# Kernel tuning notes

Hardware: AMD Instinct MI355X
Metric: run time of the kernel (lower is better)

The kernel has to match this reference:

```python
import jax, jax.numpy as jnp
import numpy as np

N_MODEL = 1024
N_HEADS = 16
KV_HEADS = 4
HEAD_DIM = N_MODEL // N_HEADS          # 64
KV_MODEL = HEAD_DIM * KV_HEADS         # 256
GROUPS = N_HEADS // KV_HEADS           # 4
B, S = 4, 2048


def _rmsnorm(x):
    return x * jax.lax.rsqrt(jnp.mean(x * x, axis=-1, keepdims=True) + 1e-6)


def _act_quant(x):
    # 8-bit absmax per-token quantization (BitNet b1.58)
    scale = 127.0 / jnp.clip(jnp.max(jnp.abs(x), axis=-1, keepdims=True), 1e-5)
    return jnp.clip(jnp.round(x * scale), -128.0, 127.0) / scale


def _weight_quant(w):
    # ternary absmean quantization
    scale = 1.0 / jnp.clip(jnp.mean(jnp.abs(w)), 1e-5)
    return jnp.clip(jnp.round(w * scale), -1.0, 1.0) / scale


def bitlinear(x, w, b):
    xn = _rmsnorm(x)
    xq = xn + jax.lax.stop_gradient(_act_quant(xn) - xn)   # STE
    wq = w + jax.lax.stop_gradient(_weight_quant(w) - w)   # STE
    return jnp.einsum('...i,oi->...o', xq, wq) + b


def setup_inputs() -> dict:
    key = jax.random.key(0)
    ks = jax.random.split(key, 11)
    sq = 1.0 / np.sqrt(N_MODEL)
    sk = 1.0 / np.sqrt(KV_MODEL)
    return {
        'query': jax.random.normal(ks[0], (B, S, N_MODEL), jnp.float32),
        'key':   jax.random.normal(ks[1], (B, S, N_MODEL), jnp.float32),
        'value': jax.random.normal(ks[2], (B, S, N_MODEL), jnp.float32),
        'Wq': jax.random.normal(ks[3], (N_MODEL, N_MODEL), jnp.float32) * sq,
        'bq': jnp.zeros((N_MODEL,), jnp.float32),
        'Wk': jax.random.normal(ks[4], (KV_MODEL, N_MODEL), jnp.float32) * sq,
        'bk': jnp.zeros((KV_MODEL,), jnp.float32),
        'Wv': jax.random.normal(ks[5], (KV_MODEL, N_MODEL), jnp.float32) * sq,
        'bv': jnp.zeros((KV_MODEL,), jnp.float32),
        'Wo': jax.random.normal(ks[6], (N_MODEL, KV_MODEL), jnp.float32) * sk,
        'bo': jnp.zeros((N_MODEL,), jnp.float32),
    }


def reference(query, key, value, Wq, bq, Wk, bk, Wv, bv, Wo, bo):
    b = query.shape[0]
    Q = bitlinear(query, Wq, bq)   # [b, n, n_model]
    K = bitlinear(key,   Wk, bk)   # [b, s, kv_model]
    V = bitlinear(value, Wv, bv)   # [b, s, kv_model]

    # [b, h, n, d] layouts
    Q = Q.reshape(b, -1, N_HEADS, HEAD_DIM).transpose(0, 2, 1, 3)
    K = K.reshape(b, -1, KV_HEADS, HEAD_DIM).transpose(0, 2, 1, 3)
    V = V.reshape(b, -1, KV_HEADS, HEAD_DIM).transpose(0, 2, 1, 3)

    # group query heads: [b, g, kv_h, n, d]
    Qg = Q.reshape(b, KV_HEADS, GROUPS, -1, HEAD_DIM).transpose(0, 2, 1, 3, 4)
    # NOTE: faithful to the module, the einsum output has no 'g' axis,
    # so the grouped query heads are SUMMED over g.
    energy = jnp.einsum('bghnd,bhsd->bhns', Qg, K)  # [b, kv_h, n, s]

    scale = jnp.sqrt(jnp.float32(HEAD_DIM))
    attention = jax.nn.softmax(energy / scale, axis=-1)
    x = jnp.einsum('bhns,bhsd->bhnd', attention, V)  # [b, kv_h, n, d]
    x = x.transpose(0, 2, 1, 3).reshape(b, -1, KV_MODEL)
    x = bitlinear(x, Wo, bo)       # [b, n, n_model]
    return (x, attention)
```

## Files before the change

kernel.cpp:

```cpp
#include <hip/hip_runtime.h>
#include <stdint.h>

#define N_MODELC 1024
#define KV_MODELC 256
#define BATCH 4
#define SEQ 2048
#define NTOK (BATCH*SEQ)

typedef __attribute__((ext_vector_type(4))) float f32x4;
typedef __attribute__((ext_vector_type(4))) int   i32x4;
typedef __attribute__((ext_vector_type(8))) short s16x8;

#define LOG2E 1.4426950408889634f
#define PSHIFT 32.0f

__device__ __forceinline__ unsigned short f2bf(float f){
  unsigned u = __builtin_bit_cast(unsigned, f);
  u = (u + 0x7FFFu + ((u>>16)&1u)) >> 16;
  return (unsigned short)u;
}
__device__ __forceinline__ float bf2f(unsigned short b){
  return __builtin_bit_cast(float, ((unsigned)b)<<16);
}

__global__ __launch_bounds__(256) void k_actquant1024(
    const float* __restrict__ xq_in, const float* __restrict__ xk_in, const float* __restrict__ xv_in,
    int8_t* __restrict__ q8q, int8_t* __restrict__ q8k, int8_t* __restrict__ q8v,
    float* __restrict__ scq, float* __restrict__ sck, float* __restrict__ scv)
{
  int row = blockIdx.x, which = blockIdx.y, t = threadIdx.x;
  const float* x = (which==0)?xq_in:(which==1)?xk_in:xv_in;
  int8_t* q8 = (which==0)?q8q:(which==1)?q8k:q8v;
  float* sc = (which==0)?scq:(which==1)?sck:scv;
  const float* xr = x + (size_t)row*N_MODELC;
  float4 v = reinterpret_cast<const float4*>(xr)[t];
  float ss = v.x*v.x + v.y*v.y + v.z*v.z + v.w*v.w;
  float am = fmaxf(fmaxf(fabsf(v.x),fabsf(v.y)), fmaxf(fabsf(v.z),fabsf(v.w)));
  #pragma unroll
  for (int m=32;m;m>>=1){ ss += __shfl_xor(ss,m,64); am = fmaxf(am, __shfl_xor(am,m,64)); }
  __shared__ float red[8];
  int wid = t>>6;
  if ((t&63)==0){ red[wid]=ss; red[4+wid]=am; }
  __syncthreads();
  ss = red[0]+red[1]+red[2]+red[3];
  am = fmaxf(fmaxf(red[4],red[5]), fmaxf(red[6],red[7]));
  float rinv = rsqrtf(ss*(1.0f/N_MODELC) + 1e-6f);
  float clipv = fmaxf(am*rinv, 1e-5f);
  float qs = 127.0f/clipv;
  float fsc = rinv*qs;
  char4 o;
  o.x = (signed char)(int)fminf(127.f, fmaxf(-128.f, rintf(v.x*fsc)));
  o.y = (signed char)(int)fminf(127.f, fmaxf(-128.f, rintf(v.y*fsc)));
  o.z = (signed char)(int)fminf(127.f, fmaxf(-128.f, rintf(v.z*fsc)));
  o.w = (signed char)(int)fminf(127.f, fmaxf(-128.f, rintf(v.w*fsc)));
  reinterpret_cast<char4*>(q8 + (size_t)row*N_MODELC)[t] = o;
  if (t==0) sc[row] = clipv*(1.0f/127.0f);
}

__global__ __launch_bounds__(64) void k_actquant256(
    const float* __restrict__ X, int8_t* __restrict__ q8, float* __restrict__ sc)
{
  int row = blockIdx.x, l = threadIdx.x;
  float4 v = reinterpret_cast<const float4*>(X + (size_t)row*KV_MODELC)[l];
  float ss = v.x*v.x + v.y*v.y + v.z*v.z + v.w*v.w;
  float am = fmaxf(fmaxf(fabsf(v.x),fabsf(v.y)), fmaxf(fabsf(v.z),fabsf(v.w)));
  #pragma unroll
  for (int m=32;m;m>>=1){ ss += __shfl_xor(ss,m,64); am = fmaxf(am, __shfl_xor(am,m,64)); }
  float rinv = rsqrtf(ss*(1.0f/KV_MODELC) + 1e-6f);
  float clipv = fmaxf(am*rinv, 1e-5f);
  float qs = 127.0f/clipv;
  float fsc = rinv*qs;
  char4 o;
  o.x = (signed char)(int)fminf(127.f, fmaxf(-128.f, rintf(v.x*fsc)));
  o.y = (signed char)(int)fminf(127.f, fmaxf(-128.f, rintf(v.y*fsc)));
  o.z = (signed char)(int)fminf(127.f, fmaxf(-128.f, rintf(v.z*fsc)));
  o.w = (signed char)(int)fminf(127.f, fmaxf(-128.f, rintf(v.w*fsc)));
  reinterpret_cast<char4*>(q8 + (size_t)row*KV_MODELC)[l] = o;
  if (l==0) sc[row] = clipv*(1.0f/127.0f);
}

__global__ __launch_bounds__(256) void k_wabs_partial(
    const float* __restrict__ Wq, const float* __restrict__ Wk,
    const float* __restrict__ Wv, const float* __restrict__ Wo, float* __restrict__ partial)
{
  int mat = blockIdx.y;
  const float* w = (mat==0)?Wq:(mat==1)?Wk:(mat==2)?Wv:Wo;
  int n = (mat==0)?(N_MODELC*N_MODELC):(KV_MODELC*N_MODELC);
  float s = 0.f;
  for (int i = blockIdx.x*256 + threadIdx.x; i < n; i += 256*256) s += fabsf(w[i]);
  #pragma unroll
  for (int m=32;m;m>>=1) s += __shfl_xor(s,m,64);
  __shared__ float red[4];
  int wid = threadIdx.x>>6;
  if ((threadIdx.x&63)==0) red[wid]=s;
  __syncthreads();
  if (threadIdx.x==0) partial[mat*256 + blockIdx.x] = red[0]+red[1]+red[2]+red[3];
}

__global__ __launch_bounds__(256) void k_wfinal(const float* __restrict__ partial, float* __restrict__ wfac)
{
  int mat = blockIdx.x, t = threadIdx.x;
  float s = partial[mat*256 + t];
  #pragma unroll
  for (int m=32;m;m>>=1) s += __shfl_xor(s,m,64);
  __shared__ float red[4];
  int wid = t>>6;
  if ((t&63)==0) red[wid]=s;
  __syncthreads();
  if (t==0){
    float tot = red[0]+red[1]+red[2]+red[3];
    float n = (mat==0)?(float)(N_MODELC*N_MODELC):(float)(KV_MODELC*N_MODELC);
    wfac[mat] = fmaxf(tot/n, 1e-5f);
  }
}

__global__ __launch_bounds__(256) void k_tern(
    const float* __restrict__ Wq, const float* __restrict__ Wk,
    const float* __restrict__ Wv, const float* __restrict__ Wo,
    const float* __restrict__ wfac,
    int8_t* __restrict__ Wqs, int8_t* __restrict__ Wkt,
    int8_t* __restrict__ Wvt, int8_t* __restrict__ Wot)
{
  int mat = blockIdx.y;
  int idx = blockIdx.x*256 + threadIdx.x;
  if (mat==0){
    float s = 1.0f/wfac[0];
    int op = idx>>10, i = idx&1023;
    int kv = op>>6, d = op&63;
    int acc = 0;
    #pragma unroll
    for (int g=0; g<4; g++){
      float w = Wq[(size_t)(kv*256 + g*64 + d)*N_MODELC + i];
      float r = fminf(1.f, fmaxf(-1.f, rintf(w*s)));
      acc += (int)r;
    }
    Wqs[idx] = (int8_t)acc;
  } else {
    const float* w = (mat==1)?Wk:(mat==2)?Wv:Wo;
    int8_t* o = (mat==1)?Wkt:(mat==2)?Wvt:Wot;
    float s = 1.0f/wfac[mat];
    float r = fminf(1.f, fmaxf(-1.f, rintf(w[idx]*s)));
    o[idx] = (int8_t)r;
  }
}

template<int MODE>
__global__ __launch_bounds__(512) void k_gemm_i8_1024(
    const int8_t* __restrict__ A, const int8_t* __restrict__ B,
    const float* __restrict__ rowscale, const float* __restrict__ wfac, int wfi,
    const float* __restrict__ bias, unsigned short* __restrict__ outp)
{
  __shared__ i32x4 redk[4][4][64];
  __shared__ unsigned short tlds[(MODE==2)?64:1][72];
  const int KDIM = 1024;
  int mb = blockIdx.x*64, nb = blockIdx.y*64;
  int w = threadIdx.x>>6, l = threadIdx.x&63, lr = l&15, lk = l>>4;
  int rw = w&3, kh = w>>2;
  const int8_t* Ap = A + (size_t)(mb + rw*16 + lr)*KDIM + kh*512 + lk*16;
  const int8_t* Bp = B + (size_t)(nb + lr)*KDIM + kh*512 + lk*16;
  i32x4 acc[4];
  #pragma unroll
  for (int f=0; f<4; f++) acc[f] = i32x4{0,0,0,0};
  #pragma unroll 4
  for (int kk=0; kk<512; kk+=64){
    i32x4 a = *reinterpret_cast<const i32x4*>(Ap + kk);
    #pragma unroll
    for (int f=0; f<4; f++){
      i32x4 b = *reinterpret_cast<const i32x4*>(Bp + (size_t)f*16*KDIM + kk);
      acc[f] = __builtin_amdgcn_mfma_i32_16x16x64_i8(a, b, acc[f], 0, 0, 0);
    }
  }
  if (kh==1){
    #pragma unroll
    for (int f=0; f<4; f++) redk[rw][f][l] = acc[f];
  }
  __syncthreads();
  if (kh==0){
    float wf = wfac[wfi];
    #pragma unroll
    for (int f=0; f<4; f++){
      acc[f] += redk[rw][f][l];
      int col = nb + f*16 + lr;
      float bval;
      if constexpr (MODE==0){
        int kv = col>>6, d = col&63;
        const float* bb = bias + kv*256 + d;
        bval = bb[0]+bb[64]+bb[128]+bb[192];
      } else {
        bval = bias[col];
      }
      #pragma unroll
      for (int r=0; r<4; r++){
        int row = mb + rw*16 + lk*4 + r;
        float val = (float)acc[f][r] * (rowscale[row]*wf) + bval;
        if constexpr (MODE==0){
          outp[(size_t)row*KV_MODELC + col] = f2bf(0.125f*val);
        } else if constexpr (MODE==1){
          outp[(size_t)row*KV_MODELC + col] = f2bf(val);
        } else {
          tlds[f*16+lr][rw*16 + lk*4 + r] = f2bf(val);
        }
      }
    }
  }
  if constexpr (MODE==2){
    __syncthreads();
    int u = threadIdx.x;
    int col = u>>3, part = u&7;
    int b = mb>>11, s0 = mb&2047;
    s16x8 vv = *reinterpret_cast<const s16x8*>(&tlds[col][part*8]);
    *reinterpret_cast<s16x8*>(&outp[((size_t)(b*256 + nb + col))*SEQ + s0 + part*8]) = vv;
  }
}

__global__ __launch_bounds__(256) void k_gemm_o(
    const int8_t* __restrict__ A, const int8_t* __restrict__ B,
    const float* __restrict__ rowscale, const float* __restrict__ wfac,
    const float* __restrict__ bias, float* __restrict__ outp)
{
  const int KDIM = 256;
  int mb = blockIdx.x*64, nb = blockIdx.y*64;
  int w = threadIdx.x>>6, l = threadIdx.x&63, lr = l&15, lk = l>>4;
  const int8_t* Ap = A + (size_t)(mb + w*16 + lr)*KDIM + lk*16;
  const int8_t* Bp = B + (size_t)(nb + lr)*KDIM + lk*16;
  i32x4 acc[4];
  #pragma unroll
  for (int f=0; f<4; f++) acc[f] = i32x4{0,0,0,0};
  #pragma unroll
  for (int kk=0; kk<KDIM; kk+=64){
    i32x4 a = *reinterpret_cast<const i32x4*>(Ap + kk);
    #pragma unroll
    for (int f=0; f<4; f++){
      i32x4 b = *reinterpret_cast<const i32x4*>(Bp + (size_t)f*16*KDIM + kk);
      acc[f] = __builtin_amdgcn_mfma_i32_16x16x64_i8(a, b, acc[f], 0, 0, 0);
    }
  }
  float wf = wfac[3];
  #pragma unroll
  for (int f=0; f<4; f++){
    int col = nb + f*16 + lr;
    float bval = bias[col];
    #pragma unroll
    for (int r=0; r<4; r++){
      int row = mb + w*16 + lk*4 + r;
      outp[(size_t)row*N_MODELC + col] = (float)acc[f][r]*(rowscale[row]*wf) + bval;
    }
  }
}

__global__ __launch_bounds__(256) void k_attn_fused(
    const unsigned short* __restrict__ Qs, const unsigned short* __restrict__ Kb,
    const unsigned short* __restrict__ VT, unsigned short* __restrict__ Pws,
    float* __restrict__ attn, float* __restrict__ X)
{
  __shared__ unsigned short plds[64][64];
  __shared__ float linvl[64];
  int bkv = blockIdx.y, b = bkv>>2, kv = bkv&3;
  int w = threadIdx.x>>6, l = threadIdx.x&63, lr = l&15, lk = l>>4;
  int brow = blockIdx.x*64;
  int rowt = brow + w*16;
  size_t tq = (size_t)(b*SEQ + rowt + lr)*KV_MODELC + kv*64 + lk*8;
  s16x8 qa0 = *reinterpret_cast<const s16x8*>(Qs + tq);
  s16x8 qa1 = *reinterpret_cast<const s16x8*>(Qs + tq + 32);
  const unsigned short* kbase = Kb + (size_t)b*SEQ*KV_MODELC + kv*64 + lk*8;
  const unsigned short* vbase = VT + ((size_t)(b*256 + kv*64))*SEQ;
  unsigned short* pblk = Pws + ((size_t)(bkv*32 + blockIdx.x))*64*SEQ;

  s16x8 ones;
  #pragma unroll
  for (int i=0;i<8;i++) ones[i] = (short)0x3F80;

  f32x4 acco[4];
  #pragma unroll
  for (int dt=0; dt<4; dt++) acco[dt] = f32x4{0.f,0.f,0.f,0.f};
  f32x4 accl = {0.f,0.f,0.f,0.f};

  int qw = w*16 + lk*4;
  int qr = w*16 + lr;
  int rsw = (lr&7)<<3;
  int rbrow = w*16 + (l>>2);
  int rbb = l&3;

  for (int st=0; st<SEQ; st+=64){
    #pragma unroll
    for (int sub=0; sub<4; sub++){
      int s0 = st + sub*16;
      const unsigned short* kp = kbase + (size_t)(s0+lr)*KV_MODELC;
      s16x8 k0 = *reinterpret_cast<const s16x8*>(kp);
      s16x8 k1 = *reinterpret_cast<const s16x8*>(kp + 32);
      f32x4 acc = {0.f,0.f,0.f,0.f};
      acc = __builtin_amdgcn_mfma_f32_16x16x32_bf16(qa0, k0, acc, 0,0,0);
      acc = __builtin_amdgcn_mfma_f32_16x16x32_bf16(qa1, k1, acc, 0,0,0);
      int slocal = sub*16 + lr;
      #pragma unroll
      for (int r=0;r<4;r++){
        float p = exp2f(fmaf(acc[r], LOG2E, -PSHIFT));
        int sw = (slocal & 7) | ((((slocal>>3) ^ ((qw+r)&7)))<<3);
        plds[qw + r][sw] = f2bf(p);
      }
    }
    s16x8 a0 = *reinterpret_cast<const s16x8*>(&plds[qr][(lk<<3) ^ rsw]);
    s16x8 a1 = *reinterpret_cast<const s16x8*>(&plds[qr][((4+lk)<<3) ^ rsw]);
    accl = __builtin_amdgcn_mfma_f32_16x16x32_bf16(a0, ones, accl, 0,0,0);
    accl = __builtin_amdgcn_mfma_f32_16x16x32_bf16(a1, ones, accl, 0,0,0);
    #pragma unroll
    for (int dt=0; dt<4; dt++){
      const unsigned short* vp = vbase + (size_t)(dt*16+lr)*SEQ + st + lk*8;
      s16x8 b0 = *reinterpret_cast<const s16x8*>(vp);
      s16x8 b1 = *reinterpret_cast<const s16x8*>(vp + 32);
      acco[dt] = __builtin_amdgcn_mfma_f32_16x16x32_bf16(a0, b0, acco[dt], 0,0,0);
      acco[dt] = __builtin_amdgcn_mfma_f32_16x16x32_bf16(a1, b1, acco[dt], 0,0,0);
    }
    unsigned short* ptile = pblk + (size_t)(st>>6)*4096;
    #pragma unroll
    for (int j8=0; j8<2; j8++){
      int chunk = rbb*2 + j8;
      s16x8 v = *reinterpret_cast<const s16x8*>(&plds[rbrow][(chunk ^ (rbrow&7))<<3]);
      *reinterpret_cast<s16x8*>(&ptile[rbrow*64 + chunk*8]) = v;
    }
  }

  float invr[4];
  #pragma unroll
  for (int r=0;r<4;r++) invr[r] = 1.0f/accl[r];
  if (lr==0){
    #pragma unroll
    for (int r=0;r<4;r++) linvl[w*16 + lk*4 + r] = invr[r];
  }
  int token = b*SEQ + rowt + lk*4;
  #pragma unroll
  for (int dt=0; dt<4; dt++){
    #pragma unroll
    for (int r=0; r<4; r++){
      X[(size_t)(token + r)*KV_MODELC + kv*64 + dt*16 + lr] = acco[dt][r]*invr[r];
    }
  }
  __syncthreads();

  float* arow = attn + (size_t)bkv*SEQ*SEQ + (size_t)brow*SEQ;
  int t = threadIdx.x;
  const unsigned short* prd = pblk + (size_t)(t>>3)*4096 + (t&7)*8;
  #pragma unroll 4
  for (int it=0; it<64; it++){
    float inv = linvl[it];
    s16x8 pv = *reinterpret_cast<const s16x8*>(prd + it*64);
    float4 o0, o1;
    o0.x = bf2f((unsigned short)pv[0])*inv;
    o0.y = bf2f((unsigned short)pv[1])*inv;
    o0.z = bf2f((unsigned short)pv[2])*inv;
    o0.w = bf2f((unsigned short)pv[3])*inv;
    o1.x = bf2f((unsigned short)pv[4])*inv;
    o1.y = bf2f((unsigned short)pv[5])*inv;
    o1.z = bf2f((unsigned short)pv[6])*inv;
    o1.w = bf2f((unsigned short)pv[7])*inv;
    float* dst = &arow[(size_t)it*SEQ + t*8];
    *reinterpret_cast<float4*>(dst) = o0;
    *reinterpret_cast<float4*>(dst+4) = o1;
  }
}

extern "C" void kernel_launch(void* const* d_in, const int* in_sizes, int n_in,
                              void* d_out, int out_size, void* d_ws, size_t ws_size,
                              hipStream_t stream)
{
  (void)in_sizes; (void)n_in; (void)out_size; (void)ws_size;
  const float* q  = (const float*)d_in[0];
  const float* k  = (const float*)d_in[1];
  const float* v  = (const float*)d_in[2];
  const float* Wq = (const float*)d_in[3];
  const float* bq = (const float*)d_in[4];
  const float* Wk = (const float*)d_in[5];
  const float* bk = (const float*)d_in[6];
  const float* Wv = (const float*)d_in[7];
  const float* bv = (const float*)d_in[8];
  const float* Wo = (const float*)d_in[9];
  const float* bo = (const float*)d_in[10];

  float* out_x = (float*)d_out;
  float* out_attn = out_x + (size_t)NTOK*N_MODELC;

  char* ws = (char*)d_ws;
  size_t off = 0;
  auto alloc = [&](size_t bytes)->void*{
    void* p = ws + off; off += (bytes + 255) & ~(size_t)255; return p;
  };
  int8_t* q8q = (int8_t*)alloc((size_t)NTOK*N_MODELC);
  int8_t* q8k = (int8_t*)alloc((size_t)NTOK*N_MODELC);
  int8_t* q8v = (int8_t*)alloc((size_t)NTOK*N_MODELC);
  int8_t* q8x = (int8_t*)alloc((size_t)NTOK*KV_MODELC);
  float* scq = (float*)alloc(NTOK*4);
  float* sck = (float*)alloc(NTOK*4);
  float* scv = (float*)alloc(NTOK*4);
  float* scx = (float*)alloc(NTOK*4);
  float* partial = (float*)alloc(4*256*4);
  float* wfac = (float*)alloc(256);
  int8_t* Wqs = (int8_t*)alloc(256*1024);
  int8_t* Wkt = (int8_t*)alloc(256*1024);
  int8_t* Wvt = (int8_t*)alloc(256*1024);
  int8_t* Wot = (int8_t*)alloc(1024*256);
  unsigned short* Qs = (unsigned short*)alloc((size_t)NTOK*KV_MODELC*2);
  unsigned short* Kb = (unsigned short*)alloc((size_t)NTOK*KV_MODELC*2);
  unsigned short* VT = (unsigned short*)alloc((size_t)NTOK*KV_MODELC*2);
  float* X = (float*)alloc((size_t)NTOK*KV_MODELC*4);
  unsigned short* Pws = (unsigned short*)alloc((size_t)16*SEQ*SEQ*2);

  hipLaunchKernelGGL(k_actquant1024, dim3(NTOK,3), dim3(256), 0, stream,
                     q,k,v, q8q,q8k,q8v, scq,sck,scv);
  hipLaunchKernelGGL(k_wabs_partial, dim3(256,4), dim3(256), 0, stream, Wq,Wk,Wv,Wo, partial);
  hipLaunchKernelGGL(k_wfinal, dim3(4), dim3(256), 0, stream, partial, wfac);
  hipLaunchKernelGGL(k_tern, dim3(1024,4), dim3(256), 0, stream,
                     Wq,Wk,Wv,Wo, wfac, Wqs,Wkt,Wvt,Wot);
  hipLaunchKernelGGL((k_gemm_i8_1024<0>), dim3(128,4), dim3(512), 0, stream,
                     q8q, Wqs, scq, wfac, 0, bq, Qs);
  hipLaunchKernelGGL((k_gemm_i8_1024<1>), dim3(128,4), dim3(512), 0, stream,
                     q8k, Wkt, sck, wfac, 1, bk, Kb);
  hipLaunchKernelGGL((k_gemm_i8_1024<2>), dim3(128,4), dim3(512), 0, stream,
                     q8v, Wvt, scv, wfac, 2, bv, VT);
  hipLaunchKernelGGL(k_attn_fused, dim3(32,16), dim3(256), 0, stream,
                     Qs, Kb, VT, Pws, out_attn, X);
  hipLaunchKernelGGL(k_actquant256, dim3(NTOK), dim3(64), 0, stream, X, q8x, scx);
  hipLaunchKernelGGL(k_gemm_o, dim3(128,16), dim3(256), 0, stream,
                     q8x, Wot, scx, wfac, bo, out_x);
}
```

Measured before the change: 351.4 us.

## Split attention over key chunks and normalize in separate reduction kernels

The fused attention kernel, which ran only 512 blocks, is split along the key dimension into 8 chunks, giving 4096 blocks. Each block writes partial row sums and partial PV accumulators, and unnormalized probabilities go to a row-major bf16 workspace. A new reduction kernel sums the partials to produce X and the inverse row sums, and a second streaming kernel rescales the workspace into the fp32 attention output. The exp2 call is also switched to the hardware builtin. The aim is better GPU occupancy, at the cost of two extra launches and extra global traffic for the partial buffers.

```diff
diff --git a/kernel.cpp b/kernel.cpp
--- a/kernel.cpp
+++ b/kernel.cpp
@@ -6,6 +6,8 @@
 #define BATCH 4
 #define SEQ 2048
 #define NTOK (BATCH*SEQ)
+#define NCHUNK 8
+#define CHUNK (SEQ/NCHUNK)
 
 typedef __attribute__((ext_vector_type(4))) float f32x4;
 typedef __attribute__((ext_vector_type(4))) int   i32x4;
@@ -248,14 +250,15 @@
   }
 }
 
-__global__ __launch_bounds__(256) void k_attn_fused(
+__global__ __launch_bounds__(256) void k_attn_a(
     const unsigned short* __restrict__ Qs, const unsigned short* __restrict__ Kb,
-    const unsigned short* __restrict__ VT, unsigned short* __restrict__ Pws,
-    float* __restrict__ attn, float* __restrict__ X)
+    const unsigned short* __restrict__ VT,
+    unsigned short* __restrict__ Pws, float* __restrict__ lpart,
+    float* __restrict__ pvpart)
 {
   __shared__ unsigned short plds[64][64];
-  __shared__ float linvl[64];
   int bkv = blockIdx.y, b = bkv>>2, kv = bkv&3;
+  int z = blockIdx.z;
   int w = threadIdx.x>>6, l = threadIdx.x&63, lr = l&15, lk = l>>4;
   int brow = blockIdx.x*64;
   int rowt = brow + w*16;
@@ -264,7 +267,6 @@
   s16x8 qa1 = *reinterpret_cast<const s16x8*>(Qs + tq + 32);
   const unsigned short* kbase = Kb + (size_t)b*SEQ*KV_MODELC + kv*64 + lk*8;
   const unsigned short* vbase = VT + ((size_t)(b*256 + kv*64))*SEQ;
-  unsigned short* pblk = Pws + ((size_t)(bkv*32 + blockIdx.x))*64*SEQ;
 
   s16x8 ones;
   #pragma unroll
@@ -281,7 +283,7 @@
   int rbrow = w*16 + (l>>2);
   int rbb = l&3;
 
-  for (int st=0; st<SEQ; st+=64){
+  for (int st=z*CHUNK; st<z*CHUNK+CHUNK; st+=64){
     #pragma unroll
     for (int sub=0; sub<4; sub++){
       int s0 = st + sub*16;
@@ -294,7 +296,7 @@
       int slocal = sub*16 + lr;
       #pragma unroll
       for (int r=0;r<4;r++){
-        float p = exp2f(fmaf(acc[r], LOG2E, -PSHIFT));
+        float p = __builtin_amdgcn_exp2f(fmaf(acc[r], LOG2E, -PSHIFT));
         int sw = (slocal & 7) | ((((slocal>>3) ^ ((qw+r)&7)))<<3);
         plds[qw + r][sw] = f2bf(p);
       }
@@ -311,49 +313,85 @@
       acco[dt] = __builtin_amdgcn_mfma_f32_16x16x32_bf16(a0, b0, acco[dt], 0,0,0);
       acco[dt] = __builtin_amdgcn_mfma_f32_16x16x32_bf16(a1, b1, acco[dt], 0,0,0);
     }
-    unsigned short* ptile = pblk + (size_t)(st>>6)*4096;
+    unsigned short* prow = Pws + ((size_t)(bkv*SEQ) + brow + rbrow)*SEQ + st;
     #pragma unroll
     for (int j8=0; j8<2; j8++){
-      int chunk = rbb*2 + j8;
-      s16x8 v = *reinterpret_cast<const s16x8*>(&plds[rbrow][(chunk ^ (rbrow&7))<<3]);
-      *reinterpret_cast<s16x8*>(&ptile[rbrow*64 + chunk*8]) = v;
-    }
-  }
-
-  float invr[4];
-  #pragma unroll
-  for (int r=0;r<4;r++) invr[r] = 1.0f/accl[r];
+      int c8 = rbb*2 + j8;
+      s16x8 vv = *reinterpret_cast<const s16x8*>(&plds[rbrow][(c8 ^ (rbrow&7))<<3]);
+      *reinterpret_cast<s16x8*>(&prow[c8*8]) = vv;
+    }
+  }
+
   if (lr==0){
     #pragma unroll
-    for (int r=0;r<4;r++) linvl[w*16 + lk*4 + r] = invr[r];
-  }
-  int token = b*SEQ + rowt + lk*4;
-  #pragma unroll
-  for (int dt=0; dt<4; dt++){
-    #pragma unroll
-    for (int r=0; r<4; r++){
-      X[(size_t)(token + r)*KV_MODELC + kv*64 + dt*16 + lr] = acco[dt][r]*invr[r];
-    }
-  }
-  __syncthreads();
-
-  float* arow = attn + (size_t)bkv*SEQ*SEQ + (size_t)brow*SEQ;
+    for (int r=0;r<4;r++)
+      lpart[((size_t)z*16 + bkv)*SEQ + rowt + lk*4 + r] = accl[r];
+  }
+  float* base = pvpart + ((((size_t)z*16 + bkv)*32 + blockIdx.x)*4 + w)*1024;
+  #pragma unroll
+  for (int dt=0; dt<4; dt++)
+    *reinterpret_cast<f32x4*>(base + (dt*64 + l)*4) = acco[dt];
+}
+
+__global__ __launch_bounds__(256) void k_pvnorm(
+    const float* __restrict__ lpart, const float* __restrict__ pvpart,
+    float* __restrict__ invl, float* __restrict__ X)
+{
+  __shared__ float xls[16][65];
+  __shared__ float linv[16];
+  int T = blockIdx.x;
+  int w = T&3, qblk = (T>>2)&31, bkv = T>>7;
+  int b = bkv>>2, kv = bkv&3;
+  int t = threadIdx.x, l = t&63, dt = t>>6, lk = l>>4, lr = l&15;
+  f32x4 s = {0.f,0.f,0.f,0.f};
+  #pragma unroll
+  for (int z=0; z<NCHUNK; z++){
+    f32x4 v = *reinterpret_cast<const f32x4*>(
+        pvpart + ((((size_t)z*16 + bkv)*32 + qblk)*4 + w)*1024 + t*4);
+    s += v;
+  }
+  if (t < 16){
+    int row = qblk*64 + w*16 + t;
+    float ls = 0.f;
+    #pragma unroll
+    for (int z=0; z<NCHUNK; z++) ls += lpart[((size_t)z*16 + bkv)*SEQ + row];
+    float iv = 1.0f/ls;
+    linv[t] = iv;
+    invl[(size_t)bkv*SEQ + row] = iv;
+  }
+  __syncthreads();
+  #pragma unroll
+  for (int r=0; r<4; r++) xls[lk*4+r][dt*16+lr] = s[r]*linv[lk*4+r];
+  __syncthreads();
+  int row = t>>4, col4 = (t&15)*4;
+  float4 o;
+  o.x = xls[row][col4];   o.y = xls[row][col4+1];
+  o.z = xls[row][col4+2]; o.w = xls[row][col4+3];
+  *reinterpret_cast<float4*>(
+      &X[((size_t)(b*SEQ + qblk*64 + w*16 + row))*KV_MODELC + kv*64 + col4]) = o;
+}
+
+__global__ __launch_bounds__(256) void k_pnorm(
+    const unsigned short* __restrict__ Pws, const float* __restrict__ invl,
+    float* __restrict__ attn)
+{
+  size_t base = (size_t)blockIdx.x*32768;
   int t = threadIdx.x;
-  const unsigned short* prd = pblk + (size_t)(t>>3)*4096 + (t&7)*8;
   #pragma unroll 4
-  for (int it=0; it<64; it++){
-    float inv = linvl[it];
-    s16x8 pv = *reinterpret_cast<const s16x8*>(prd + it*64);
+  for (int i=0; i<16; i++){
+    size_t idx = base + (size_t)i*2048 + t*8;
+    float iv = invl[idx>>11];
+    s16x8 pv = *reinterpret_cast<const s16x8*>(&Pws[idx]);
     float4 o0, o1;
-    o0.x = bf2f((unsigned short)pv[0])*inv;
-    o0.y = bf2f((unsigned short)pv[1])*inv;
-    o0.z = bf2f((unsigned short)pv[2])*inv;
-    o0.w = bf2f((unsigned short)pv[3])*inv;
-    o1.x = bf2f((unsigned short)pv[4])*inv;
-    o1.y = bf2f((unsigned short)pv[5])*inv;
-    o1.z = bf2f((unsigned short)pv[6])*inv;
-    o1.w = bf2f((unsigned short)pv[7])*inv;
-    float* dst = &arow[(size_t)it*SEQ + t*8];
+    o0.x = bf2f((unsigned short)pv[0])*iv;
+    o0.y = bf2f((unsigned short)pv[1])*iv;
+    o0.z = bf2f((unsigned short)pv[2])*iv;
+    o0.w = bf2f((unsigned short)pv[3])*iv;
+    o1.x = bf2f((unsigned short)pv[4])*iv;
+    o1.y = bf2f((unsigned short)pv[5])*iv;
+    o1.z = bf2f((unsigned short)pv[6])*iv;
+    o1.w = bf2f((unsigned short)pv[7])*iv;
+    float* dst = &attn[idx];
     *reinterpret_cast<float4*>(dst) = o0;
     *reinterpret_cast<float4*>(dst+4) = o1;
   }
@@ -403,6 +441,9 @@
   unsigned short* VT = (unsigned short*)alloc((size_t)NTOK*KV_MODELC*2);
   float* X = (float*)alloc((size_t)NTOK*KV_MODELC*4);
   unsigned short* Pws = (unsigned short*)alloc((size_t)16*SEQ*SEQ*2);
+  float* lpart = (float*)alloc((size_t)NCHUNK*16*SEQ*4);
+  float* pvpart = (float*)alloc((size_t)NCHUNK*16*32*4*1024*4);
+  float* invl = (float*)alloc((size_t)16*SEQ*4);
 
   hipLaunchKernelGGL(k_actquant1024, dim3(NTOK,3), dim3(256), 0, stream,
                      q,k,v, q8q,q8k,q8v, scq,sck,scv);
@@ -416,8 +457,12 @@
                      q8k, Wkt, sck, wfac, 1, bk, Kb);
   hipLaunchKernelGGL((k_gemm_i8_1024<2>), dim3(128,4), dim3(512), 0, stream,
                      q8v, Wvt, scv, wfac, 2, bv, VT);
-  hipLaunchKernelGGL(k_attn_fused, dim3(32,16), dim3(256), 0, stream,
-                     Qs, Kb, VT, Pws, out_attn, X);
+  hipLaunchKernelGGL(k_attn_a, dim3(32,16,NCHUNK), dim3(256), 0, stream,
+                     Qs, Kb, VT, Pws, lpart, pvpart);
+  hipLaunchKernelGGL(k_pvnorm, dim3(2048), dim3(256), 0, stream,
+                     lpart, pvpart, invl, X);
+  hipLaunchKernelGGL(k_pnorm, dim3(2048), dim3(256), 0, stream,
+                     Pws, invl, out_attn);
   hipLaunchKernelGGL(k_actquant256, dim3(NTOK), dim3(64), 0, stream, X, q8x, scx);
   hipLaunchKernelGGL(k_gemm_o, dim3(128,16), dim3(256), 0, stream,
                      q8x, Wot, scx, wfac, bo, out_x);
```

Result: slower. 373.7 us (+6.3%).

## Recompute attention scores in second pass instead of spilling bf16 probabilities

Applied to the files above, without the earlier changes.

The attention kernel no longer writes unnormalized bf16 probabilities to a large workspace and reads them back. It runs a second QK^T pass after the row sums are known and writes normalized fp32 attention directly. Q/K/V projection outputs are stored in per-head contiguous layouts, with V pre-tiled in 64x64 blocks. Blocks shrink to 128 threads covering 32 query rows, so there are twice as many blocks. This removes roughly 256MB of workspace traffic at the cost of doubling the QK MFMA and exp work.

```diff
diff --git a/kernel.cpp b/kernel.cpp
--- a/kernel.cpp
+++ b/kernel.cpp
@@ -10,6 +10,7 @@
 typedef __attribute__((ext_vector_type(4))) float f32x4;
 typedef __attribute__((ext_vector_type(4))) int   i32x4;
 typedef __attribute__((ext_vector_type(8))) short s16x8;
+typedef __attribute__((ext_vector_type(4))) short s16x4;
 
 #define LOG2E 1.4426950408889634f
 #define PSHIFT 32.0f
@@ -194,9 +195,11 @@
         int row = mb + rw*16 + lk*4 + r;
         float val = (float)acc[f][r] * (rowscale[row]*wf) + bval;
         if constexpr (MODE==0){
-          outp[(size_t)row*KV_MODELC + col] = f2bf(0.125f*val);
+          int bb2 = row>>11, s = row&2047, kvh = col>>6, d = col&63;
+          outp[(((size_t)(bb2*4+kvh))*SEQ + s)*64 + d] = f2bf(0.125f*val);
         } else if constexpr (MODE==1){
-          outp[(size_t)row*KV_MODELC + col] = f2bf(val);
+          int bb2 = row>>11, s = row&2047, kvh = col>>6, d = col&63;
+          outp[(((size_t)(bb2*4+kvh))*SEQ + s)*64 + d] = f2bf(val);
         } else {
           tlds[f*16+lr][rw*16 + lk*4 + r] = f2bf(val);
         }
@@ -208,8 +211,10 @@
     int u = threadIdx.x;
     int col = u>>3, part = u&7;
     int b = mb>>11, s0 = mb&2047;
+    int bkv = b*4 + blockIdx.y, sT = s0>>6;
     s16x8 vv = *reinterpret_cast<const s16x8*>(&tlds[col][part*8]);
-    *reinterpret_cast<s16x8*>(&outp[((size_t)(b*256 + nb + col))*SEQ + s0 + part*8]) = vv;
+    *reinterpret_cast<s16x8*>(
+        &outp[(((size_t)(bkv*32 + sT))*64 + col)*64 + part*8]) = vv;
   }
 }
 
@@ -248,23 +253,20 @@
   }
 }
 
-__global__ __launch_bounds__(256) void k_attn_fused(
-    const unsigned short* __restrict__ Qs, const unsigned short* __restrict__ Kb,
-    const unsigned short* __restrict__ VT, unsigned short* __restrict__ Pws,
+__global__ __launch_bounds__(128) void k_attn_full(
+    const unsigned short* __restrict__ Qh, const unsigned short* __restrict__ Kh,
+    const unsigned short* __restrict__ Vh,
     float* __restrict__ attn, float* __restrict__ X)
 {
-  __shared__ unsigned short plds[64][64];
-  __shared__ float linvl[64];
+  __shared__ unsigned short plds[2][16][64];
   int bkv = blockIdx.y, b = bkv>>2, kv = bkv&3;
   int w = threadIdx.x>>6, l = threadIdx.x&63, lr = l&15, lk = l>>4;
-  int brow = blockIdx.x*64;
-  int rowt = brow + w*16;
-  size_t tq = (size_t)(b*SEQ + rowt + lr)*KV_MODELC + kv*64 + lk*8;
-  s16x8 qa0 = *reinterpret_cast<const s16x8*>(Qs + tq);
-  s16x8 qa1 = *reinterpret_cast<const s16x8*>(Qs + tq + 32);
-  const unsigned short* kbase = Kb + (size_t)b*SEQ*KV_MODELC + kv*64 + lk*8;
-  const unsigned short* vbase = VT + ((size_t)(b*256 + kv*64))*SEQ;
-  unsigned short* pblk = Pws + ((size_t)(bkv*32 + blockIdx.x))*64*SEQ;
+  int rowt = blockIdx.x*32 + w*16;
+  size_t tq = ((size_t)bkv*SEQ + rowt + lr)*64 + lk*8;
+  s16x8 qa0 = *reinterpret_cast<const s16x8*>(Qh + tq);
+  s16x8 qa1 = *reinterpret_cast<const s16x8*>(Qh + tq + 32);
+  const unsigned short* kbase = Kh + (size_t)bkv*SEQ*64 + lk*8;
+  const unsigned short* vbase = Vh + (size_t)bkv*32*4096 + lk*8;
 
   s16x8 ones;
   #pragma unroll
@@ -275,17 +277,14 @@
   for (int dt=0; dt<4; dt++) acco[dt] = f32x4{0.f,0.f,0.f,0.f};
   f32x4 accl = {0.f,0.f,0.f,0.f};
 
-  int qw = w*16 + lk*4;
-  int qr = w*16 + lr;
-  int rsw = (lr&7)<<3;
-  int rbrow = w*16 + (l>>2);
-  int rbb = l&3;
+  int qwl = lk*4;
+  int rswl = (lr&7)<<3;
 
   for (int st=0; st<SEQ; st+=64){
     #pragma unroll
     for (int sub=0; sub<4; sub++){
       int s0 = st + sub*16;
-      const unsigned short* kp = kbase + (size_t)(s0+lr)*KV_MODELC;
+      const unsigned short* kp = kbase + (size_t)(s0+lr)*64;
       s16x8 k0 = *reinterpret_cast<const s16x8*>(kp);
       s16x8 k1 = *reinterpret_cast<const s16x8*>(kp + 32);
       f32x4 acc = {0.f,0.f,0.f,0.f};
@@ -294,40 +293,30 @@
       int slocal = sub*16 + lr;
       #pragma unroll
       for (int r=0;r<4;r++){
-        float p = exp2f(fmaf(acc[r], LOG2E, -PSHIFT));
-        int sw = (slocal & 7) | ((((slocal>>3) ^ ((qw+r)&7)))<<3);
-        plds[qw + r][sw] = f2bf(p);
+        float p = __builtin_amdgcn_exp2f(fmaf(acc[r], LOG2E, -PSHIFT));
+        int sw = (slocal & 7) | ((((slocal>>3) ^ ((qwl+r)&7)))<<3);
+        plds[w][qwl + r][sw] = f2bf(p);
       }
     }
-    s16x8 a0 = *reinterpret_cast<const s16x8*>(&plds[qr][(lk<<3) ^ rsw]);
-    s16x8 a1 = *reinterpret_cast<const s16x8*>(&plds[qr][((4+lk)<<3) ^ rsw]);
+    s16x8 a0 = *reinterpret_cast<const s16x8*>(&plds[w][lr][(lk<<3) ^ rswl]);
+    s16x8 a1 = *reinterpret_cast<const s16x8*>(&plds[w][lr][((4+lk)<<3) ^ rswl]);
     accl = __builtin_amdgcn_mfma_f32_16x16x32_bf16(a0, ones, accl, 0,0,0);
     accl = __builtin_amdgcn_mfma_f32_16x16x32_bf16(a1, ones, accl, 0,0,0);
+    const unsigned short* vt = vbase + (size_t)(st>>6)*4096;
     #pragma unroll
     for (int dt=0; dt<4; dt++){
-      const unsigned short* vp = vbase + (size_t)(dt*16+lr)*SEQ + st + lk*8;
+      const unsigned short* vp = vt + (size_t)(dt*16+lr)*64;
       s16x8 b0 = *reinterpret_cast<const s16x8*>(vp);
       s16x8 b1 = *reinterpret_cast<const s16x8*>(vp + 32);
       acco[dt] = __builtin_amdgcn_mfma_f32_16x16x32_bf16(a0, b0, acco[dt], 0,0,0);
       acco[dt] = __builtin_amdgcn_mfma_f32_16x16x32_bf16(a1, b1, acco[dt], 0,0,0);
     }
-    unsigned short* ptile = pblk + (size_t)(st>>6)*4096;
-    #pragma unroll
-    for (int j8=0; j8<2; j8++){
-      int chunk = rbb*2 + j8;
-      s16x8 v = *reinterpret_cast<const s16x8*>(&plds[rbrow][(chunk ^ (rbrow&7))<<3]);
-      *reinterpret_cast<s16x8*>(&ptile[rbrow*64 + chunk*8]) = v;
-    }
   }
 
   float invr[4];
   #pragma unroll
   for (int r=0;r<4;r++) invr[r] = 1.0f/accl[r];
-  if (lr==0){
-    #pragma unroll
-    for (int r=0;r<4;r++) linvl[w*16 + lk*4 + r] = invr[r];
-  }
-  int token = b*SEQ + rowt + lk*4;
+  int token = b*SEQ + rowt + qwl;
   #pragma unroll
   for (int dt=0; dt<4; dt++){
     #pragma unroll
@@ -335,27 +324,40 @@
       X[(size_t)(token + r)*KV_MODELC + kv*64 + dt*16 + lr] = acco[dt][r]*invr[r];
     }
   }
-  __syncthreads();
-
-  float* arow = attn + (size_t)bkv*SEQ*SEQ + (size_t)brow*SEQ;
-  int t = threadIdx.x;
-  const unsigned short* prd = pblk + (size_t)(t>>3)*4096 + (t&7)*8;
-  #pragma unroll 4
-  for (int it=0; it<64; it++){
-    float inv = linvl[it];
-    s16x8 pv = *reinterpret_cast<const s16x8*>(prd + it*64);
-    float4 o0, o1;
-    o0.x = bf2f((unsigned short)pv[0])*inv;
-    o0.y = bf2f((unsigned short)pv[1])*inv;
-    o0.z = bf2f((unsigned short)pv[2])*inv;
-    o0.w = bf2f((unsigned short)pv[3])*inv;
-    o1.x = bf2f((unsigned short)pv[4])*inv;
-    o1.y = bf2f((unsigned short)pv[5])*inv;
-    o1.z = bf2f((unsigned short)pv[6])*inv;
-    o1.w = bf2f((unsigned short)pv[7])*inv;
-    float* dst = &arow[(size_t)it*SEQ + t*8];
-    *reinterpret_cast<float4*>(dst) = o0;
-    *reinterpret_cast<float4*>(dst+4) = o1;
+
+  float* arow = attn + (size_t)bkv*SEQ*SEQ + (size_t)rowt*SEQ;
+  for (int st=0; st<SEQ; st+=64){
+    #pragma unroll
+    for (int sub=0; sub<4; sub++){
+      int s0 = st + sub*16;
+      const unsigned short* kp = kbase + (size_t)(s0+lr)*64;
+      s16x8 k0 = *reinterpret_cast<const s16x8*>(kp);
+      s16x8 k1 = *reinterpret_cast<const s16x8*>(kp + 32);
+      f32x4 acc = {0.f,0.f,0.f,0.f};
+      acc = __builtin_amdgcn_mfma_f32_16x16x32_bf16(qa0, k0, acc, 0,0,0);
+      acc = __builtin_amdgcn_mfma_f32_16x16x32_bf16(qa1, k1, acc, 0,0,0);
+      int slocal = sub*16 + lr;
+      #pragma unroll
+      for (int r=0;r<4;r++){
+        float p = __builtin_amdgcn_exp2f(fmaf(acc[r], LOG2E, -PSHIFT))*invr[r];
+        int sw = (slocal & 7) | ((((slocal>>3) ^ ((qwl+r)&7)))<<3);
+        plds[w][qwl + r][sw] = f2bf(p);
+      }
+    }
+    #pragma unroll
+    for (int j=0; j<4; j++){
+      int rowl = j*4 + (l>>4);
+      int sseg = l & 15;
+      int chunk = sseg >> 1, half = sseg & 1;
+      int off = ((chunk ^ (rowl&7)) << 3) + (half<<2);
+      s16x4 pb = *reinterpret_cast<const s16x4*>(&plds[w][rowl][off]);
+      float4 o;
+      o.x = bf2f((unsigned short)pb[0]);
+      o.y = bf2f((unsigned short)pb[1]);
+      o.z = bf2f((unsigned short)pb[2]);
+      o.w = bf2f((unsigned short)pb[3]);
+      *reinterpret_cast<float4*>(&arow[(size_t)rowl*SEQ + st + sseg*4]) = o;
+    }
   }
 }
 
@@ -398,11 +400,10 @@
   int8_t* Wkt = (int8_t*)alloc(256*1024);
   int8_t* Wvt = (int8_t*)alloc(256*1024);
   int8_t* Wot = (int8_t*)alloc(1024*256);
-  unsigned short* Qs = (unsigned short*)alloc((size_t)NTOK*KV_MODELC*2);
-  unsigned short* Kb = (unsigned short*)alloc((size_t)NTOK*KV_MODELC*2);
-  unsigned short* VT = (unsigned short*)alloc((size_t)NTOK*KV_MODELC*2);
+  unsigned short* Qh = (unsigned short*)alloc((size_t)NTOK*KV_MODELC*2);
+  unsigned short* Kh = (unsigned short*)alloc((size_t)NTOK*KV_MODELC*2);
+  unsigned short* Vh = (unsigned short*)alloc((size_t)NTOK*KV_MODELC*2);
   float* X = (float*)alloc((size_t)NTOK*KV_MODELC*4);
-  unsigned short* Pws = (unsigned short*)alloc((size_t)16*SEQ*SEQ*2);
 
   hipLaunchKernelGGL(k_actquant1024, dim3(NTOK,3), dim3(256), 0, stream,
                      q,k,v, q8q,q8k,q8v, scq,sck,scv);
@@ -411,13 +412,13 @@
   hipLaunchKernelGGL(k_tern, dim3(1024,4), dim3(256), 0, stream,
                      Wq,Wk,Wv,Wo, wfac, Wqs,Wkt,Wvt,Wot);
   hipLaunchKernelGGL((k_gemm_i8_1024<0>), dim3(128,4), dim3(512), 0, stream,
-                     q8q, Wqs, scq, wfac, 0, bq, Qs);
+                     q8q, Wqs, scq, wfac, 0, bq, Qh);
   hipLaunchKernelGGL((k_gemm_i8_1024<1>), dim3(128,4), dim3(512), 0, stream,
-                     q8k, Wkt, sck, wfac, 1, bk, Kb);
+                     q8k, Wkt, sck, wfac, 1, bk, Kh);
   hipLaunchKernelGGL((k_gemm_i8_1024<2>), dim3(128,4), dim3(512), 0, stream,
-                     q8v, Wvt, scv, wfac, 2, bv, VT);
-  hipLaunchKernelGGL(k_attn_fused, dim3(32,16), dim3(256), 0, stream,
-                     Qs, Kb, VT, Pws, out_attn, X);
+                     q8v, Wvt, scv, wfac, 2, bv, Vh);
+  hipLaunchKernelGGL(k_attn_full, dim3(64,16), dim3(128), 0, stream,
+                     Qh, Kh, Vh, out_attn, X);
   hipLaunchKernelGGL(k_actquant256, dim3(NTOK), dim3(64), 0, stream, X, q8x, scx);
   hipLaunchKernelGGL(k_gemm_o, dim3(128,16), dim3(256), 0, stream,
                      q8x, Wot, scx, wfac, bo, out_x);
```

New measurement: 319.8 us. -9.0%, faster.
